# Optimization experiments

Hardware: AMD Instinct MI355X
Metric: run time of the kernel (lower is better)

Reference implementation:

```python
import jax, jax.numpy as jnp
import numpy as np
import math


def setup_inputs() -> dict:
    key = jax.random.key(0)
    ks = jax.random.split(key, 16)
    B, S, H, K, PREV = 32, 2048, 1024, 4, 2
    sc = 0.02
    return {
        "last_hidden": jax.random.normal(ks[0], (1, B, H), jnp.float32),
        "decoder_inputs": jax.random.normal(ks[1], (B, 1, H), jnp.float32),
        "encoder_outputs": jax.random.normal(ks[2], (B, S, H), jnp.float32),
        "attention_scores": jax.random.normal(ks[3], (PREV, B, 1, S), jnp.float32),
        "attention_mask": jnp.zeros((B, 1, S), jnp.float32),
        "evidence_scores": jax.random.uniform(ks[4], (B,), jnp.float32),
        "evidence_sentence_index": jax.random.randint(ks[5], (B, PREV), 0, S, dtype=jnp.int32),
        "W_ih": jax.random.normal(ks[6], (3 * H, H), jnp.float32) * sc,
        "W_hh": jax.random.normal(ks[7], (3 * H, H), jnp.float32) * sc,
        "b_ih": jax.random.normal(ks[8], (3 * H,), jnp.float32) * sc,
        "b_hh": jax.random.normal(ks[9], (3 * H,), jnp.float32) * sc,
        "Wk": jax.random.normal(ks[10], (H, H), jnp.float32) * sc,
        "bk": jnp.zeros((H,), jnp.float32),
        "Wv": jax.random.normal(ks[11], (H, H), jnp.float32) * sc,
        "bv": jnp.zeros((H,), jnp.float32),
        "topk": K,
    }


def _gru_step(x, h, W_ih, W_hh, b_ih, b_hh):
    # x, h: (B, H). PyTorch GRU cell math.
    gi = x @ W_ih.T + b_ih  # (B, 3H)
    gh = h @ W_hh.T + b_hh  # (B, 3H)
    i_r, i_z, i_n = jnp.split(gi, 3, axis=1)
    h_r, h_z, h_n = jnp.split(gh, 3, axis=1)
    r = jax.nn.sigmoid(i_r + h_r)
    z = jax.nn.sigmoid(i_z + h_z)
    n = jnp.tanh(i_n + r * h_n)
    return (1.0 - z) * n + z * h


def reference(last_hidden, decoder_inputs, encoder_outputs, attention_scores,
              attention_mask, evidence_scores, evidence_sentence_index,
              W_ih, W_hh, b_ih, b_hh, Wk, bk, Wv, bv, topk):
    B, S, H = encoder_outputs.shape
    K = topk
    R = B // K  # real batch (beam groups)

    key_eo = encoder_outputs @ Wk.T + bk    # (B, S, H)
    val_eo = encoder_outputs @ Wv.T + bv    # (B, S, H)

    h_new = _gru_step(decoder_inputs[:, 0], last_hidden[0], W_ih, W_hh, b_ih, b_hh)  # (B, H)
    output = h_new[:, None, :]              # (B, 1, H)

    attn_outputs = jnp.einsum('bih,bsh->bis', output, key_eo) / math.sqrt(H) + attention_mask  # (B,1,S)
    attn_alignment = jax.nn.softmax(attn_outputs, axis=-1)
    context = jnp.einsum('bis,bsh->bih', attn_alignment, val_eo)  # (B, 1, H)

    # top-k per beam, then joint rerank over topk*topk candidates per real example
    vals, idx = jax.lax.top_k(attn_alignment.reshape(R, K, S), K)  # (R, K, K), sorted desc
    scores = vals.reshape(B, K)
    sentences = idx.reshape(B, K)
    log_scores = -jnp.log(scores) + evidence_scores[:, None]       # (B, K)

    flat = log_scores.reshape(R, K * K)
    order = jnp.argsort(flat, axis=-1)[:, :K]                      # (R, K) ascending, stable
    new_evidence_scores = jnp.take_along_axis(flat, order, axis=1).reshape(B)
    s_flat = (order // K + jnp.arange(R)[:, None] * K).reshape(B)  # source beam in [0, B)
    r_flat = (order % K).reshape(B)

    sel_sent = sentences[s_flat, r_flat]                           # (B,)
    result = context[s_flat]                                       # (B, 1, H)
    hidden = h_new[s_flat][None]                                   # (1, B, H)
    new_evidence_sentence_index = jnp.concatenate(
        [evidence_sentence_index[s_flat], sel_sent[:, None].astype(evidence_sentence_index.dtype)], axis=1)
    new_attention_scores = jnp.concatenate(
        [attention_scores[:, s_flat], attn_outputs[s_flat][None]], axis=0)  # (prev+1, B, 1, S)
    new_attention_mask = attention_mask[s_flat]                    # (B, 1, S)

    return (result, hidden, new_evidence_sentence_index,
            new_attention_scores, new_attention_mask, new_evidence_scores)
```

## Files before the change

### kernel.cpp

```cpp
#include <hip/hip_runtime.h>
#include <hip/hip_bf16.h>
#include <cfloat>
#include <climits>
#include <cmath>

#define BB 32
#define SS 2048
#define HH 1024
#define KK 4
#define CH 32

__global__ __launch_bounds__(256) void gates_partial(
    const float* __restrict__ x, const float* __restrict__ h_old,
    const float* __restrict__ W_ih, const float* __restrict__ W_hh,
    float* __restrict__ part) {
  int t = threadIdx.x;
  int jb = blockIdx.x;
  int k0 = blockIdx.y * 64;
  bool second = (jb >= 12);
  const float* A = second ? h_old : x;
  const float* W = second ? W_hh : W_ih;
  int j0 = jb * 256;
  int jr = j0 - (second ? 3072 : 0);
  const float* wp = W + (size_t)(jr + t) * HH + k0;
  float acc[32];
#pragma unroll
  for (int b = 0; b < 32; b++) acc[b] = 0.f;
  for (int kk = 0; kk < 64; kk += 4) {
    float4 wv = *(const float4*)(wp + kk);
#pragma unroll
    for (int b = 0; b < 32; b++) {
      float4 a = *(const float4*)(A + (size_t)b * HH + k0 + kk);
      acc[b] += a.x * wv.x + a.y * wv.y + a.z * wv.z + a.w * wv.w;
    }
  }
  float* pb = part + (size_t)blockIdx.y * (32 * 6144) + j0 + t;
#pragma unroll
  for (int b = 0; b < 32; b++) pb[(size_t)b * 6144] = acc[b];
}

__global__ __launch_bounds__(256) void gates_reduce_gru(
    const float* __restrict__ part, const float* __restrict__ b_ih,
    const float* __restrict__ b_hh, const float* __restrict__ h_old,
    float* __restrict__ h_new) {
  int t = threadIdx.x;
  int b = blockIdx.x >> 2;
  int h = (blockIdx.x & 3) * 256 + t;
  float s0 = 0.f, s1 = 0.f, s2 = 0.f, s3 = 0.f, s4 = 0.f, s5 = 0.f;
#pragma unroll
  for (int kc = 0; kc < 16; kc++) {
    const float* p = part + ((size_t)kc * 32 + b) * 6144;
    s0 += p[h];
    s1 += p[1024 + h];
    s2 += p[2048 + h];
    s3 += p[3072 + h];
    s4 += p[4096 + h];
    s5 += p[5120 + h];
  }
  float ir = s0 + b_ih[h], iz = s1 + b_ih[1024 + h], in_ = s2 + b_ih[2048 + h];
  float hr = s3 + b_hh[h], hz = s4 + b_hh[1024 + h], hn = s5 + b_hh[2048 + h];
  float r = 1.f / (1.f + expf(-(ir + hr)));
  float z = 1.f / (1.f + expf(-(iz + hz)));
  float n = tanhf(in_ + r * hn);
  h_new[b * HH + h] = (1.f - z) * n + z * h_old[b * HH + h];
}

__global__ __launch_bounds__(256) void q_partial(const float* __restrict__ hnew,
                                                 const float* __restrict__ Wk,
                                                 float* __restrict__ qpart) {
  int t = threadIdx.x;
  int n0 = blockIdx.x * 512 + 2 * t;
  int k0 = blockIdx.y * 32;
  float acc0[32], acc1[32];
#pragma unroll
  for (int b = 0; b < 32; b++) { acc0[b] = 0.f; acc1[b] = 0.f; }
  for (int k = 0; k < 32; k += 4) {
    float2 w0 = *(const float2*)(Wk + (size_t)(k0 + k) * HH + n0);
    float2 w1 = *(const float2*)(Wk + (size_t)(k0 + k + 1) * HH + n0);
    float2 w2 = *(const float2*)(Wk + (size_t)(k0 + k + 2) * HH + n0);
    float2 w3 = *(const float2*)(Wk + (size_t)(k0 + k + 3) * HH + n0);
#pragma unroll
    for (int b = 0; b < 32; b++) {
      float4 a = *(const float4*)(hnew + (size_t)b * HH + k0 + k);
      acc0[b] += a.x * w0.x + a.y * w1.x + a.z * w2.x + a.w * w3.x;
      acc1[b] += a.x * w0.y + a.y * w1.y + a.z * w2.y + a.w * w3.y;
    }
  }
  float* pb = qpart + (size_t)blockIdx.y * (32 * 1024) + n0;
#pragma unroll
  for (int b = 0; b < 32; b++)
    *(float2*)(pb + (size_t)b * 1024) = make_float2(acc0[b], acc1[b]);
}

__global__ __launch_bounds__(256) void q_reduce_hbk(
    const float* __restrict__ qpart, const float* __restrict__ hnew,
    const float* __restrict__ bk, float* __restrict__ q,
    float* __restrict__ hbk) {
  int t = threadIdx.x;
  if (blockIdx.x < 128) {
    int b = blockIdx.x >> 2;
    int n = (blockIdx.x & 3) * 256 + t;
    float s = 0.f;
#pragma unroll
    for (int kc = 0; kc < 32; kc++) s += qpart[((size_t)kc * 32 + b) * 1024 + n];
    q[b * HH + n] = s;
  } else {
    int w = t >> 6, lane = t & 63;
    const float4* bk4 = (const float4*)bk;
    float4 kv[4];
#pragma unroll
    for (int i = 0; i < 4; i++) kv[i] = bk4[i * 64 + lane];
    for (int b = w; b < BB; b += 4) {
      const float4* h4 = (const float4*)(hnew + (size_t)b * HH);
      float s = 0.f;
#pragma unroll
      for (int i = 0; i < 4; i++) {
        float4 hv = h4[i * 64 + lane];
        s += hv.x * kv[i].x + hv.y * kv[i].y + hv.z * kv[i].z + hv.w * kv[i].w;
      }
#pragma unroll
      for (int off = 32; off; off >>= 1) s += __shfl_xor(s, off);
      if (lane == 0) hbk[b] = s;
    }
  }
}

__global__ __launch_bounds__(256, 4) void fused_attn(
    const float* __restrict__ eo, const float* __restrict__ q,
    const float* __restrict__ hbk, const float* __restrict__ mask,
    float* __restrict__ logits, float* __restrict__ c0part,
    float* __restrict__ msum_part) {
  __shared__ float cacc[4][1024];
  __shared__ float cms[4][2];
  int b = blockIdx.y, sc = blockIdx.x, t = threadIdx.x;
  int w = t >> 6, lane = t & 63;
  const float4* q4 = (const float4*)(q + (size_t)b * HH);
  float4 qv[4];
#pragma unroll
  for (int i = 0; i < 4; i++) qv[i] = q4[i * 64 + lane];
  float hb = hbk[b];
  float m = -FLT_MAX, sum = 0.f;
  float4 acc[4];
#pragma unroll
  for (int i = 0; i < 4; i++) acc[i] = make_float4(0.f, 0.f, 0.f, 0.f);
  int rbase = sc * 64 + w * 16;
  for (int tile = 0; tile < 8; tile++) {
    int r0 = rbase + tile * 2;
    float4 rv[2][4];
#pragma unroll
    for (int rr = 0; rr < 2; rr++) {
      const float4* e4 = (const float4*)(eo + ((size_t)b * SS + r0 + rr) * HH);
#pragma unroll
      for (int i = 0; i < 4; i++) rv[rr][i] = e4[i * 64 + lane];
    }
    float p0 = 0.f, p1 = 0.f;
#pragma unroll
    for (int i = 0; i < 4; i++) {
      p0 += rv[0][i].x * qv[i].x + rv[0][i].y * qv[i].y +
            rv[0][i].z * qv[i].z + rv[0][i].w * qv[i].w;
      p1 += rv[1][i].x * qv[i].x + rv[1][i].y * qv[i].y +
            rv[1][i].z * qv[i].z + rv[1][i].w * qv[i].w;
    }
#pragma unroll
    for (int off = 32; off; off >>= 1) {
      p0 += __shfl_xor(p0, off);
      p1 += __shfl_xor(p1, off);
    }
    float lv0 = (p0 + hb) * 0.03125f + mask[(size_t)b * SS + r0];
    float lv1 = (p1 + hb) * 0.03125f + mask[(size_t)b * SS + r0 + 1];
    if (lane == 0) {
      logits[(size_t)b * SS + r0] = lv0;
      logits[(size_t)b * SS + r0 + 1] = lv1;
    }
    float m_new = fmaxf(m, fmaxf(lv0, lv1));
    float scale = expf(m - m_new);
    float w0 = expf(lv0 - m_new), w1 = expf(lv1 - m_new);
    sum = sum * scale + w0 + w1;
#pragma unroll
    for (int i = 0; i < 4; i++) {
      acc[i].x = acc[i].x * scale + w0 * rv[0][i].x + w1 * rv[1][i].x;
      acc[i].y = acc[i].y * scale + w0 * rv[0][i].y + w1 * rv[1][i].y;
      acc[i].z = acc[i].z * scale + w0 * rv[0][i].z + w1 * rv[1][i].z;
      acc[i].w = acc[i].w * scale + w0 * rv[0][i].w + w1 * rv[1][i].w;
    }
    m = m_new;
  }
#pragma unroll
  for (int i = 0; i < 4; i++)
    *(float4*)&cacc[w][i * 256 + lane * 4] = acc[i];
  if (lane == 0) { cms[w][0] = m; cms[w][1] = sum; }
  __syncthreads();
  float m0 = cms[0][0], m1 = cms[1][0], m2 = cms[2][0], m3 = cms[3][0];
  float mb = fmaxf(fmaxf(m0, m1), fmaxf(m2, m3));
  float wt0 = expf(m0 - mb), wt1 = expf(m1 - mb), wt2 = expf(m2 - mb),
        wt3 = expf(m3 - mb);
  float sb = cms[0][1] * wt0 + cms[1][1] * wt1 + cms[2][1] * wt2 + cms[3][1] * wt3;
  float4 a0 = *(float4*)&cacc[0][4 * t];
  float4 a1 = *(float4*)&cacc[1][4 * t];
  float4 a2 = *(float4*)&cacc[2][4 * t];
  float4 a3 = *(float4*)&cacc[3][4 * t];
  float4 r;
  r.x = wt0 * a0.x + wt1 * a1.x + wt2 * a2.x + wt3 * a3.x;
  r.y = wt0 * a0.y + wt1 * a1.y + wt2 * a2.y + wt3 * a3.y;
  r.z = wt0 * a0.z + wt1 * a1.z + wt2 * a2.z + wt3 * a3.z;
  r.w = wt0 * a0.w + wt1 * a1.w + wt2 * a2.w + wt3 * a3.w;
  *(float4*)(c0part + ((size_t)sc * 32 + b) * 1024 + 4 * t) = r;
  if (t == 0) {
    msum_part[((size_t)sc * 32 + b) * 2 + 0] = mb;
    msum_part[((size_t)sc * 32 + b) * 2 + 1] = sb;
  }
}

__device__ __forceinline__ bool vi_better(float av, int ai, float bv, int bi) {
  return av > bv || (av == bv && ai < bi);
}

__global__ __launch_bounds__(256) void attn_finish(
    const float* __restrict__ c0part, const float* __restrict__ msum_part,
    const float* __restrict__ logits, float* __restrict__ c0,
    float* __restrict__ scores, int* __restrict__ sent) {
  int b = blockIdx.x, t = threadIdx.x;
  float m = -FLT_MAX;
  float ms[CH];
#pragma unroll
  for (int c = 0; c < CH; c++) {
    ms[c] = msum_part[((size_t)c * 32 + b) * 2 + 0];
    m = fmaxf(m, ms[c]);
  }
  float sum = 0.f;
  float wc[CH];
#pragma unroll
  for (int c = 0; c < CH; c++) {
    wc[c] = expf(ms[c] - m);
    sum += msum_part[((size_t)c * 32 + b) * 2 + 1] * wc[c];
  }
  float inv = 1.f / sum;
  float4 a = make_float4(0.f, 0.f, 0.f, 0.f);
#pragma unroll
  for (int c = 0; c < CH; c++) {
    float4 v = *(const float4*)(c0part + ((size_t)c * 32 + b) * 1024 + 4 * t);
    a.x += wc[c] * v.x; a.y += wc[c] * v.y;
    a.z += wc[c] * v.z; a.w += wc[c] * v.w;
  }
  a.x *= inv; a.y *= inv; a.z *= inv; a.w *= inv;
  *(float4*)(c0 + (size_t)b * HH + 4 * t) = a;

  float tv0 = -FLT_MAX, tv1 = -FLT_MAX, tv2 = -FLT_MAX, tv3 = -FLT_MAX;
  int ti0 = INT_MAX, ti1 = INT_MAX, ti2 = INT_MAX, ti3 = INT_MAX;
#pragma unroll
  for (int it = 0; it < 8; it++) {
    int idx = it * 256 + t;
    float v = logits[(size_t)b * SS + idx];
    if (vi_better(v, idx, tv3, ti3)) {
      tv3 = v; ti3 = idx;
      if (vi_better(tv3, ti3, tv2, ti2)) { float fv = tv2; int fi = ti2; tv2 = tv3; ti2 = ti3; tv3 = fv; ti3 = fi; }
      if (vi_better(tv2, ti2, tv1, ti1)) { float fv = tv1; int fi = ti1; tv1 = tv2; ti1 = ti2; tv2 = fv; ti2 = fi; }
      if (vi_better(tv1, ti1, tv0, ti0)) { float fv = tv0; int fi = ti0; tv0 = tv1; ti0 = ti1; tv1 = fv; ti1 = fi; }
    }
  }
  __shared__ float sv[256][4];
  __shared__ int si[256][4];
  sv[t][0] = tv0; sv[t][1] = tv1; sv[t][2] = tv2; sv[t][3] = tv3;
  si[t][0] = ti0; si[t][1] = ti1; si[t][2] = ti2; si[t][3] = ti3;
  __syncthreads();
  for (int off = 128; off; off >>= 1) {
    if (t < off) {
      float bv0 = sv[t + off][0], bv1 = sv[t + off][1], bv2 = sv[t + off][2], bv3 = sv[t + off][3];
      int bi0 = si[t + off][0], bi1 = si[t + off][1], bi2 = si[t + off][2], bi3 = si[t + off][3];
      float mv0, mv1, mv2, mv3; int mi0, mi1, mi2, mi3;
      if (vi_better(tv0, ti0, bv3, bi3)) { mv0 = tv0; mi0 = ti0; } else { mv0 = bv3; mi0 = bi3; }
      if (vi_better(tv1, ti1, bv2, bi2)) { mv1 = tv1; mi1 = ti1; } else { mv1 = bv2; mi1 = bi2; }
      if (vi_better(tv2, ti2, bv1, bi1)) { mv2 = tv2; mi2 = ti2; } else { mv2 = bv1; mi2 = bi1; }
      if (vi_better(tv3, ti3, bv0, bi0)) { mv3 = tv3; mi3 = ti3; } else { mv3 = bv0; mi3 = bi0; }
      if (!vi_better(mv0, mi0, mv2, mi2)) { float fv = mv0; int fi = mi0; mv0 = mv2; mi0 = mi2; mv2 = fv; mi2 = fi; }
      if (!vi_better(mv1, mi1, mv3, mi3)) { float fv = mv1; int fi = mi1; mv1 = mv3; mi1 = mi3; mv3 = fv; mi3 = fi; }
      if (!vi_better(mv0, mi0, mv1, mi1)) { float fv = mv0; int fi = mi0; mv0 = mv1; mi0 = mi1; mv1 = fv; mi1 = fi; }
      if (!vi_better(mv2, mi2, mv3, mi3)) { float fv = mv2; int fi = mi2; mv2 = mv3; mi2 = mi3; mv3 = fv; mi3 = fi; }
      tv0 = mv0; tv1 = mv1; tv2 = mv2; tv3 = mv3;
      ti0 = mi0; ti1 = mi1; ti2 = mi2; ti3 = mi3;
      sv[t][0] = tv0; sv[t][1] = tv1; sv[t][2] = tv2; sv[t][3] = tv3;
      si[t][0] = ti0; si[t][1] = ti1; si[t][2] = ti2; si[t][3] = ti3;
    }
    __syncthreads();
  }
  if (t == 0) {
    scores[b * KK + 0] = expf(tv0 - m) * inv; sent[b * KK + 0] = ti0;
    scores[b * KK + 1] = expf(tv1 - m) * inv; sent[b * KK + 1] = ti1;
    scores[b * KK + 2] = expf(tv2 - m) * inv; sent[b * KK + 2] = ti2;
    scores[b * KK + 3] = expf(tv3 - m) * inv; sent[b * KK + 3] = ti3;
  }
}

__global__ __launch_bounds__(256) void ctx_partial(const float* __restrict__ c0,
                                                   const float* __restrict__ Wv,
                                                   float* __restrict__ part) {
  int t = threadIdx.x;
  int j = blockIdx.x * 256 + t;
  int k0 = blockIdx.y * 32;
  const float* wp = Wv + (size_t)j * HH + k0;
  float acc[32];
#pragma unroll
  for (int b = 0; b < 32; b++) acc[b] = 0.f;
  for (int kk = 0; kk < 32; kk += 4) {
    float4 wv = *(const float4*)(wp + kk);
#pragma unroll
    for (int b = 0; b < 32; b++) {
      float4 a = *(const float4*)(c0 + (size_t)b * HH + k0 + kk);
      acc[b] += a.x * wv.x + a.y * wv.y + a.z * wv.z + a.w * wv.w;
    }
  }
  float* pb = part + (size_t)blockIdx.y * (32 * 1024) + j;
#pragma unroll
  for (int b = 0; b < 32; b++) pb[(size_t)b * 1024] = acc[b];
}

__global__ __launch_bounds__(256) void sel_gather(
    const float* __restrict__ scores, const int* __restrict__ sent,
    const float* __restrict__ evidence, const int* __restrict__ esi,
    const float* __restrict__ ctxpart, const float* __restrict__ bv,
    const float* __restrict__ hnew, const float* __restrict__ attn_in,
    const float* __restrict__ logits, const float* __restrict__ mask,
    float* __restrict__ out0, float* __restrict__ out1,
    float* __restrict__ out2, float* __restrict__ out3,
    float* __restrict__ out4, float* __restrict__ out5) {
  __shared__ int s_sh;
  int b = blockIdx.x, t = threadIdx.x;
  if (t == 0) {
    int r = b >> 2, j = b & 3;
    float ls[16];
    bool used[16];
    for (int k1 = 0; k1 < 4; k1++)
      for (int k2 = 0; k2 < 4; k2++)
        ls[k1 * 4 + k2] = -logf(scores[(r * 4 + k1) * 4 + k2]) + evidence[r * 4 + k1];
    for (int i = 0; i < 16; i++) used[i] = false;
    int best = 0;
    float bvv = FLT_MAX;
    for (int jj = 0; jj <= j; jj++) {
      best = 0;
      bvv = FLT_MAX;
      for (int i = 0; i < 16; i++)
        if (!used[i] && ls[i] < bvv) { bvv = ls[i]; best = i; }
      used[best] = true;
    }
    int k1 = best >> 2, k2 = best & 3;
    int sSel = r * 4 + k1;
    s_sh = sSel;
    out5[b] = bvv;
    out2[b * 3 + 0] = (float)esi[sSel * 2 + 0];
    out2[b * 3 + 1] = (float)esi[sSel * 2 + 1];
    out2[b * 3 + 2] = (float)sent[sSel * 4 + k2];
  }
  __syncthreads();
  int s = s_sh;
  {
    float4 s0 = ((const float4*)bv)[t];
#pragma unroll
    for (int kc = 0; kc < 32; kc++) {
      float4 v = *(const float4*)(ctxpart + ((size_t)kc * 32 + s) * 1024 + 4 * t);
      s0.x += v.x; s0.y += v.y; s0.z += v.z; s0.w += v.w;
    }
    ((float4*)(out0 + (size_t)b * HH))[t] = s0;
    ((float4*)(out1 + (size_t)b * HH))[t] =
        ((const float4*)(hnew + (size_t)s * HH))[t];
  }
#pragma unroll
  for (int p = 0; p < 2; p++) {
    const float4* src = (const float4*)(attn_in + ((size_t)p * BB + s) * SS);
    float4* dst = (float4*)(out3 + ((size_t)p * BB + b) * SS);
    dst[t] = src[t];
    dst[t + 256] = src[t + 256];
  }
  {
    const float4* lg = (const float4*)(logits + (size_t)s * SS);
    float4* d2 = (float4*)(out3 + ((size_t)2 * BB + b) * SS);
    d2[t] = lg[t];
    d2[t + 256] = lg[t + 256];
    const float4* mk = (const float4*)(mask + (size_t)s * SS);
    float4* d4 = (float4*)(out4 + (size_t)b * SS);
    d4[t] = mk[t];
    d4[t + 256] = mk[t + 256];
  }
}

extern "C" void kernel_launch(void* const* d_in, const int* in_sizes, int n_in,
                              void* d_out, int out_size, void* d_ws, size_t ws_size,
                              hipStream_t stream) {
  const float* h_old = (const float*)d_in[0];
  const float* x     = (const float*)d_in[1];
  const float* eo    = (const float*)d_in[2];
  const float* attn_in = (const float*)d_in[3];
  const float* mask  = (const float*)d_in[4];
  const float* evidence = (const float*)d_in[5];
  const int*   esi   = (const int*)d_in[6];
  const float* W_ih  = (const float*)d_in[7];
  const float* W_hh  = (const float*)d_in[8];
  const float* b_ih  = (const float*)d_in[9];
  const float* b_hh  = (const float*)d_in[10];
  const float* Wk    = (const float*)d_in[11];
  const float* bk    = (const float*)d_in[12];
  const float* Wv    = (const float*)d_in[13];
  const float* bv    = (const float*)d_in[14];

  float* w = (float*)d_ws;
  float* h_new  = w + 0;
  float* q      = w + 32768;
  float* hbk    = w + 65536;
  float* logits = w + 65568;
  float* scores = w + 131104;
  int*   sent   = (int*)(w + 131232);
  float* c0     = w + 131360;
  float* msum_part = w + 164128;
  float* c0part = w + 166176;
  float* gpart  = w + 1214752;
  float* qpart  = w + 4360480;
  float* ctxpart= w + 5409056;

  float* out0 = (float*)d_out;
  float* out1 = out0 + 32768;
  float* out2 = out1 + 32768;
  float* out3 = out2 + 96;
  float* out4 = out3 + 196608;
  float* out5 = out4 + 65536;

  gates_partial<<<dim3(24, 16), 256, 0, stream>>>(x, h_old, W_ih, W_hh, gpart);
  gates_reduce_gru<<<128, 256, 0, stream>>>(gpart, b_ih, b_hh, h_old, h_new);
  q_partial<<<dim3(2, 32), 256, 0, stream>>>(h_new, Wk, qpart);
  q_reduce_hbk<<<129, 256, 0, stream>>>(qpart, h_new, bk, q, hbk);
  fused_attn<<<dim3(CH, BB), 256, 0, stream>>>(eo, q, hbk, mask, logits, c0part, msum_part);
  attn_finish<<<BB, 256, 0, stream>>>(c0part, msum_part, logits, c0, scores, sent);
  ctx_partial<<<dim3(4, 32), 256, 0, stream>>>(c0, Wv, ctxpart);
  sel_gather<<<BB, 256, 0, stream>>>(scores, sent, evidence, esi, ctxpart, bv,
                                     h_new, attn_in, logits, mask,
                                     out0, out1, out2, out3, out4, out5);
}
```

Before: 153.6 us.

## Fuse GRU with query projection, fold q-reduce into attention, fuse ctx GEMV into gather

Merges the GRU reduction with the Wk query projection into one kernel that writes 4 per-chunk partials. The q reduction and the h·bk bias dot now happen at the start of fused_attn, staged through LDS. The context Wv projection is computed only for each selected beam inside the gather kernel, which replaces a separate all-batch GEMV and its partial reduction. The attention loop is also software-pipelined with double-buffered row tiles. Together this cuts the launch count from 8 to 5 and removes intermediate partial buffers. The cost is that fused_attn reads the q partials redundantly in every block, and the per-beam Wv GEMV reads Wv once per output beam.

New measurement: 238.7 us. 55.5% more time.

```diff
diff --git a/kernel.cpp b/kernel.cpp
--- a/kernel.cpp
+++ b/kernel.cpp
@@ -39,17 +39,19 @@
   for (int b = 0; b < 32; b++) pb[(size_t)b * 6144] = acc[b];
 }
 
-__global__ __launch_bounds__(256) void gates_reduce_gru(
+__global__ __launch_bounds__(256) void gru_q(
     const float* __restrict__ part, const float* __restrict__ b_ih,
     const float* __restrict__ b_hh, const float* __restrict__ h_old,
-    float* __restrict__ h_new) {
+    const float* __restrict__ Wk, float* __restrict__ h_new,
+    float* __restrict__ qpart2) {
+  __shared__ float hs[256];
   int t = threadIdx.x;
-  int b = blockIdx.x >> 2;
-  int h = (blockIdx.x & 3) * 256 + t;
+  int kc = blockIdx.x, b = blockIdx.y;
+  int h = kc * 256 + t;
   float s0 = 0.f, s1 = 0.f, s2 = 0.f, s3 = 0.f, s4 = 0.f, s5 = 0.f;
 #pragma unroll
-  for (int kc = 0; kc < 16; kc++) {
-    const float* p = part + ((size_t)kc * 32 + b) * 6144;
+  for (int c = 0; c < 16; c++) {
+    const float* p = part + ((size_t)c * 32 + b) * 6144;
     s0 += p[h];
     s1 += p[1024 + h];
     s2 += p[2048 + h];
@@ -62,132 +64,123 @@
   float r = 1.f / (1.f + expf(-(ir + hr)));
   float z = 1.f / (1.f + expf(-(iz + hz)));
   float n = tanhf(in_ + r * hn);
-  h_new[b * HH + h] = (1.f - z) * n + z * h_old[b * HH + h];
-}
-
-__global__ __launch_bounds__(256) void q_partial(const float* __restrict__ hnew,
-                                                 const float* __restrict__ Wk,
-                                                 float* __restrict__ qpart) {
-  int t = threadIdx.x;
-  int n0 = blockIdx.x * 512 + 2 * t;
-  int k0 = blockIdx.y * 32;
-  float acc0[32], acc1[32];
-#pragma unroll
-  for (int b = 0; b < 32; b++) { acc0[b] = 0.f; acc1[b] = 0.f; }
-  for (int k = 0; k < 32; k += 4) {
-    float2 w0 = *(const float2*)(Wk + (size_t)(k0 + k) * HH + n0);
-    float2 w1 = *(const float2*)(Wk + (size_t)(k0 + k + 1) * HH + n0);
-    float2 w2 = *(const float2*)(Wk + (size_t)(k0 + k + 2) * HH + n0);
-    float2 w3 = *(const float2*)(Wk + (size_t)(k0 + k + 3) * HH + n0);
-#pragma unroll
-    for (int b = 0; b < 32; b++) {
-      float4 a = *(const float4*)(hnew + (size_t)b * HH + k0 + k);
-      acc0[b] += a.x * w0.x + a.y * w1.x + a.z * w2.x + a.w * w3.x;
-      acc1[b] += a.x * w0.y + a.y * w1.y + a.z * w2.y + a.w * w3.y;
-    }
-  }
-  float* pb = qpart + (size_t)blockIdx.y * (32 * 1024) + n0;
-#pragma unroll
-  for (int b = 0; b < 32; b++)
-    *(float2*)(pb + (size_t)b * 1024) = make_float2(acc0[b], acc1[b]);
-}
-
-__global__ __launch_bounds__(256) void q_reduce_hbk(
-    const float* __restrict__ qpart, const float* __restrict__ hnew,
-    const float* __restrict__ bk, float* __restrict__ q,
-    float* __restrict__ hbk) {
-  int t = threadIdx.x;
-  if (blockIdx.x < 128) {
-    int b = blockIdx.x >> 2;
-    int n = (blockIdx.x & 3) * 256 + t;
-    float s = 0.f;
-#pragma unroll
-    for (int kc = 0; kc < 32; kc++) s += qpart[((size_t)kc * 32 + b) * 1024 + n];
-    q[b * HH + n] = s;
-  } else {
-    int w = t >> 6, lane = t & 63;
-    const float4* bk4 = (const float4*)bk;
-    float4 kv[4];
-#pragma unroll
-    for (int i = 0; i < 4; i++) kv[i] = bk4[i * 64 + lane];
-    for (int b = w; b < BB; b += 4) {
-      const float4* h4 = (const float4*)(hnew + (size_t)b * HH);
-      float s = 0.f;
-#pragma unroll
-      for (int i = 0; i < 4; i++) {
-        float4 hv = h4[i * 64 + lane];
-        s += hv.x * kv[i].x + hv.y * kv[i].y + hv.z * kv[i].z + hv.w * kv[i].w;
-      }
-#pragma unroll
-      for (int off = 32; off; off >>= 1) s += __shfl_xor(s, off);
-      if (lane == 0) hbk[b] = s;
-    }
-  }
+  float hv = (1.f - z) * n + z * h_old[b * HH + h];
+  h_new[b * HH + h] = hv;
+  hs[t] = hv;
+  __syncthreads();
+  float4 acc = make_float4(0.f, 0.f, 0.f, 0.f);
+  const float* wbase = Wk + (size_t)kc * 256 * HH + 4 * t;
+  for (int k = 0; k < 256; k += 4) {
+    float4 w0 = *(const float4*)(wbase + (size_t)(k + 0) * HH);
+    float4 w1 = *(const float4*)(wbase + (size_t)(k + 1) * HH);
+    float4 w2 = *(const float4*)(wbase + (size_t)(k + 2) * HH);
+    float4 w3 = *(const float4*)(wbase + (size_t)(k + 3) * HH);
+    float a0 = hs[k], a1 = hs[k + 1], a2 = hs[k + 2], a3 = hs[k + 3];
+    acc.x += a0 * w0.x + a1 * w1.x + a2 * w2.x + a3 * w3.x;
+    acc.y += a0 * w0.y + a1 * w1.y + a2 * w2.y + a3 * w3.y;
+    acc.z += a0 * w0.z + a1 * w1.z + a2 * w2.z + a3 * w3.z;
+    acc.w += a0 * w0.w + a1 * w1.w + a2 * w2.w + a3 * w3.w;
+  }
+  *(float4*)(qpart2 + ((size_t)b * 4 + kc) * HH + 4 * t) = acc;
+}
+
+__device__ __forceinline__ void attn_load_tile(float4 (&rv)[2][4],
+                                               const float* __restrict__ eo,
+                                               int b, int r0, int lane) {
+#pragma unroll
+  for (int rr = 0; rr < 2; rr++) {
+    const float4* e4 = (const float4*)(eo + ((size_t)b * SS + r0 + rr) * HH);
+#pragma unroll
+    for (int i = 0; i < 4; i++) rv[rr][i] = e4[i * 64 + lane];
+  }
+}
+
+__device__ __forceinline__ void attn_process_tile(
+    const float4 (&rv)[2][4], const float4 (&qv)[4], float hb,
+    const float* __restrict__ mask, float* __restrict__ logits, int b, int r0,
+    int lane, float& m, float& sum, float4 (&acc)[4]) {
+  float p0 = 0.f, p1 = 0.f;
+#pragma unroll
+  for (int i = 0; i < 4; i++) {
+    p0 += rv[0][i].x * qv[i].x + rv[0][i].y * qv[i].y +
+          rv[0][i].z * qv[i].z + rv[0][i].w * qv[i].w;
+    p1 += rv[1][i].x * qv[i].x + rv[1][i].y * qv[i].y +
+          rv[1][i].z * qv[i].z + rv[1][i].w * qv[i].w;
+  }
+#pragma unroll
+  for (int off = 32; off; off >>= 1) {
+    p0 += __shfl_xor(p0, off);
+    p1 += __shfl_xor(p1, off);
+  }
+  float lv0 = (p0 + hb) * 0.03125f + mask[(size_t)b * SS + r0];
+  float lv1 = (p1 + hb) * 0.03125f + mask[(size_t)b * SS + r0 + 1];
+  if (lane == 0) {
+    logits[(size_t)b * SS + r0] = lv0;
+    logits[(size_t)b * SS + r0 + 1] = lv1;
+  }
+  float m_new = fmaxf(m, fmaxf(lv0, lv1));
+  float scale = expf(m - m_new);
+  float w0 = expf(lv0 - m_new), w1 = expf(lv1 - m_new);
+  sum = sum * scale + w0 + w1;
+#pragma unroll
+  for (int i = 0; i < 4; i++) {
+    acc[i].x = acc[i].x * scale + w0 * rv[0][i].x + w1 * rv[1][i].x;
+    acc[i].y = acc[i].y * scale + w0 * rv[0][i].y + w1 * rv[1][i].y;
+    acc[i].z = acc[i].z * scale + w0 * rv[0][i].z + w1 * rv[1][i].z;
+    acc[i].w = acc[i].w * scale + w0 * rv[0][i].w + w1 * rv[1][i].w;
+  }
+  m = m_new;
 }
 
 __global__ __launch_bounds__(256, 4) void fused_attn(
-    const float* __restrict__ eo, const float* __restrict__ q,
-    const float* __restrict__ hbk, const float* __restrict__ mask,
-    float* __restrict__ logits, float* __restrict__ c0part,
-    float* __restrict__ msum_part) {
+    const float* __restrict__ eo, const float* __restrict__ qpart2,
+    const float* __restrict__ h_new, const float* __restrict__ bk,
+    const float* __restrict__ mask, float* __restrict__ logits,
+    float* __restrict__ c0part, float* __restrict__ msum_part) {
+  __shared__ float q_lds[HH];
+  __shared__ float wred[4];
   __shared__ float cacc[4][1024];
   __shared__ float cms[4][2];
   int b = blockIdx.y, sc = blockIdx.x, t = threadIdx.x;
   int w = t >> 6, lane = t & 63;
-  const float4* q4 = (const float4*)(q + (size_t)b * HH);
+  {
+    float4 qs = *(const float4*)(qpart2 + ((size_t)b * 4 + 0) * HH + 4 * t);
+#pragma unroll
+    for (int kc = 1; kc < 4; kc++) {
+      float4 v = *(const float4*)(qpart2 + ((size_t)b * 4 + kc) * HH + 4 * t);
+      qs.x += v.x; qs.y += v.y; qs.z += v.z; qs.w += v.w;
+    }
+    *(float4*)&q_lds[4 * t] = qs;
+    float4 hv = *(const float4*)(h_new + (size_t)b * HH + 4 * t);
+    float4 kv = *(const float4*)(bk + 4 * t);
+    float p = hv.x * kv.x + hv.y * kv.y + hv.z * kv.z + hv.w * kv.w;
+#pragma unroll
+    for (int off = 32; off; off >>= 1) p += __shfl_xor(p, off);
+    if (lane == 0) wred[w] = p;
+  }
+  __syncthreads();
+  float hb = wred[0] + wred[1] + wred[2] + wred[3];
   float4 qv[4];
 #pragma unroll
-  for (int i = 0; i < 4; i++) qv[i] = q4[i * 64 + lane];
-  float hb = hbk[b];
+  for (int i = 0; i < 4; i++) qv[i] = *(const float4*)&q_lds[(i * 64 + lane) * 4];
+
   float m = -FLT_MAX, sum = 0.f;
   float4 acc[4];
 #pragma unroll
   for (int i = 0; i < 4; i++) acc[i] = make_float4(0.f, 0.f, 0.f, 0.f);
   int rbase = sc * 64 + w * 16;
-  for (int tile = 0; tile < 8; tile++) {
-    int r0 = rbase + tile * 2;
-    float4 rv[2][4];
-#pragma unroll
-    for (int rr = 0; rr < 2; rr++) {
-      const float4* e4 = (const float4*)(eo + ((size_t)b * SS + r0 + rr) * HH);
-#pragma unroll
-      for (int i = 0; i < 4; i++) rv[rr][i] = e4[i * 64 + lane];
-    }
-    float p0 = 0.f, p1 = 0.f;
-#pragma unroll
-    for (int i = 0; i < 4; i++) {
-      p0 += rv[0][i].x * qv[i].x + rv[0][i].y * qv[i].y +
-            rv[0][i].z * qv[i].z + rv[0][i].w * qv[i].w;
-      p1 += rv[1][i].x * qv[i].x + rv[1][i].y * qv[i].y +
-            rv[1][i].z * qv[i].z + rv[1][i].w * qv[i].w;
-    }
-#pragma unroll
-    for (int off = 32; off; off >>= 1) {
-      p0 += __shfl_xor(p0, off);
-      p1 += __shfl_xor(p1, off);
-    }
-    float lv0 = (p0 + hb) * 0.03125f + mask[(size_t)b * SS + r0];
-    float lv1 = (p1 + hb) * 0.03125f + mask[(size_t)b * SS + r0 + 1];
-    if (lane == 0) {
-      logits[(size_t)b * SS + r0] = lv0;
-      logits[(size_t)b * SS + r0 + 1] = lv1;
-    }
-    float m_new = fmaxf(m, fmaxf(lv0, lv1));
-    float scale = expf(m - m_new);
-    float w0 = expf(lv0 - m_new), w1 = expf(lv1 - m_new);
-    sum = sum * scale + w0 + w1;
-#pragma unroll
-    for (int i = 0; i < 4; i++) {
-      acc[i].x = acc[i].x * scale + w0 * rv[0][i].x + w1 * rv[1][i].x;
-      acc[i].y = acc[i].y * scale + w0 * rv[0][i].y + w1 * rv[1][i].y;
-      acc[i].z = acc[i].z * scale + w0 * rv[0][i].z + w1 * rv[1][i].z;
-      acc[i].w = acc[i].w * scale + w0 * rv[0][i].w + w1 * rv[1][i].w;
-    }
-    m = m_new;
-  }
-#pragma unroll
-  for (int i = 0; i < 4; i++)
-    *(float4*)&cacc[w][i * 256 + lane * 4] = acc[i];
+  float4 rvA[2][4], rvB[2][4];
+  attn_load_tile(rvA, eo, b, rbase, lane);
+#pragma unroll 1
+  for (int it = 0; it < 4; it++) {
+    int r0 = rbase + it * 4;
+    attn_load_tile(rvB, eo, b, r0 + 2, lane);
+    attn_process_tile(rvA, qv, hb, mask, logits, b, r0, lane, m, sum, acc);
+    if (it < 3) attn_load_tile(rvA, eo, b, r0 + 4, lane);
+    attn_process_tile(rvB, qv, hb, mask, logits, b, r0 + 2, lane, m, sum, acc);
+  }
+#pragma unroll
+  for (int i = 0; i < 4; i++) *(float4*)&cacc[w][i * 256 + lane * 4] = acc[i];
   if (lane == 0) { cms[w][0] = m; cms[w][1] = sum; }
   __syncthreads();
   float m0 = cms[0][0], m1 = cms[1][0], m2 = cms[2][0], m3 = cms[3][0];
@@ -291,40 +284,19 @@
   }
 }
 
-__global__ __launch_bounds__(256) void ctx_partial(const float* __restrict__ c0,
-                                                   const float* __restrict__ Wv,
-                                                   float* __restrict__ part) {
-  int t = threadIdx.x;
-  int j = blockIdx.x * 256 + t;
-  int k0 = blockIdx.y * 32;
-  const float* wp = Wv + (size_t)j * HH + k0;
-  float acc[32];
-#pragma unroll
-  for (int b = 0; b < 32; b++) acc[b] = 0.f;
-  for (int kk = 0; kk < 32; kk += 4) {
-    float4 wv = *(const float4*)(wp + kk);
-#pragma unroll
-    for (int b = 0; b < 32; b++) {
-      float4 a = *(const float4*)(c0 + (size_t)b * HH + k0 + kk);
-      acc[b] += a.x * wv.x + a.y * wv.y + a.z * wv.z + a.w * wv.w;
-    }
-  }
-  float* pb = part + (size_t)blockIdx.y * (32 * 1024) + j;
-#pragma unroll
-  for (int b = 0; b < 32; b++) pb[(size_t)b * 1024] = acc[b];
-}
-
-__global__ __launch_bounds__(256) void sel_gather(
+__global__ __launch_bounds__(256) void ctx_sel_gather(
     const float* __restrict__ scores, const int* __restrict__ sent,
     const float* __restrict__ evidence, const int* __restrict__ esi,
-    const float* __restrict__ ctxpart, const float* __restrict__ bv,
-    const float* __restrict__ hnew, const float* __restrict__ attn_in,
-    const float* __restrict__ logits, const float* __restrict__ mask,
-    float* __restrict__ out0, float* __restrict__ out1,
-    float* __restrict__ out2, float* __restrict__ out3,
-    float* __restrict__ out4, float* __restrict__ out5) {
+    const float* __restrict__ Wv, const float* __restrict__ bvec,
+    const float* __restrict__ c0, const float* __restrict__ hnew,
+    const float* __restrict__ attn_in, const float* __restrict__ logits,
+    const float* __restrict__ mask, float* __restrict__ out0,
+    float* __restrict__ out1, float* __restrict__ out2,
+    float* __restrict__ out3, float* __restrict__ out4,
+    float* __restrict__ out5) {
   __shared__ int s_sh;
-  int b = blockIdx.x, t = threadIdx.x;
+  int jq = blockIdx.x, b = blockIdx.y, t = threadIdx.x;
+  int w = t >> 6, lane = t & 63;
   if (t == 0) {
     int r = b >> 2, j = b & 3;
     float ls[16];
@@ -345,41 +317,43 @@
     int k1 = best >> 2, k2 = best & 3;
     int sSel = r * 4 + k1;
     s_sh = sSel;
-    out5[b] = bvv;
-    out2[b * 3 + 0] = (float)esi[sSel * 2 + 0];
-    out2[b * 3 + 1] = (float)esi[sSel * 2 + 1];
-    out2[b * 3 + 2] = (float)sent[sSel * 4 + k2];
+    if (jq == 0) {
+      out5[b] = bvv;
+      out2[b * 3 + 0] = (float)esi[sSel * 2 + 0];
+      out2[b * 3 + 1] = (float)esi[sSel * 2 + 1];
+      out2[b * 3 + 2] = (float)sent[sSel * 4 + k2];
+    }
   }
   __syncthreads();
   int s = s_sh;
-  {
-    float4 s0 = ((const float4*)bv)[t];
-#pragma unroll
-    for (int kc = 0; kc < 32; kc++) {
-      float4 v = *(const float4*)(ctxpart + ((size_t)kc * 32 + s) * 1024 + 4 * t);
-      s0.x += v.x; s0.y += v.y; s0.z += v.z; s0.w += v.w;
-    }
-    ((float4*)(out0 + (size_t)b * HH))[t] = s0;
-    ((float4*)(out1 + (size_t)b * HH))[t] =
-        ((const float4*)(hnew + (size_t)s * HH))[t];
-  }
+  float4 cv[4];
+  const float4* c4 = (const float4*)(c0 + (size_t)s * HH);
+#pragma unroll
+  for (int i = 0; i < 4; i++) cv[i] = c4[i * 64 + lane];
+  int jbase = jq * 256 + w * 64;
+  for (int rr = 0; rr < 64; rr++) {
+    int j = jbase + rr;
+    const float4* w4 = (const float4*)(Wv + (size_t)j * HH);
+    float p = 0.f;
+#pragma unroll
+    for (int i = 0; i < 4; i++) {
+      float4 wv = w4[i * 64 + lane];
+      p += wv.x * cv[i].x + wv.y * cv[i].y + wv.z * cv[i].z + wv.w * cv[i].w;
+    }
+#pragma unroll
+    for (int off = 32; off; off >>= 1) p += __shfl_xor(p, off);
+    if (lane == 0) out0[(size_t)b * HH + j] = p + bvec[j];
+  }
+  out1[(size_t)b * HH + jq * 256 + t] = hnew[(size_t)s * HH + jq * 256 + t];
 #pragma unroll
   for (int p = 0; p < 2; p++) {
-    const float4* src = (const float4*)(attn_in + ((size_t)p * BB + s) * SS);
-    float4* dst = (float4*)(out3 + ((size_t)p * BB + b) * SS);
-    dst[t] = src[t];
-    dst[t + 256] = src[t + 256];
-  }
-  {
-    const float4* lg = (const float4*)(logits + (size_t)s * SS);
-    float4* d2 = (float4*)(out3 + ((size_t)2 * BB + b) * SS);
-    d2[t] = lg[t];
-    d2[t + 256] = lg[t + 256];
-    const float4* mk = (const float4*)(mask + (size_t)s * SS);
-    float4* d4 = (float4*)(out4 + (size_t)b * SS);
-    d4[t] = mk[t];
-    d4[t + 256] = mk[t + 256];
-  }
+    *(float2*)(out3 + ((size_t)p * BB + b) * SS + jq * 512 + 2 * t) =
+        *(const float2*)(attn_in + ((size_t)p * BB + s) * SS + jq * 512 + 2 * t);
+  }
+  *(float2*)(out3 + ((size_t)2 * BB + b) * SS + jq * 512 + 2 * t) =
+      *(const float2*)(logits + (size_t)s * SS + jq * 512 + 2 * t);
+  *(float2*)(out4 + (size_t)b * SS + jq * 512 + 2 * t) =
+      *(const float2*)(mask + (size_t)s * SS + jq * 512 + 2 * t);
 }
 
 extern "C" void kernel_launch(void* const* d_in, const int* in_sizes, int n_in,
@@ -403,17 +377,14 @@
 
   float* w = (float*)d_ws;
   float* h_new  = w + 0;
-  float* q      = w + 32768;
-  float* hbk    = w + 65536;
-  float* logits = w + 65568;
-  float* scores = w + 131104;
-  int*   sent   = (int*)(w + 131232);
-  float* c0     = w + 131360;
-  float* msum_part = w + 164128;
-  float* c0part = w + 166176;
-  float* gpart  = w + 1214752;
-  float* qpart  = w + 4360480;
-  float* ctxpart= w + 5409056;
+  float* logits = w + 32768;
+  float* scores = w + 98304;
+  int*   sent   = (int*)(w + 98432);
+  float* c0     = w + 98560;
+  float* msum_part = w + 131328;
+  float* c0part = w + 133376;
+  float* gpart  = w + 1181952;
+  float* qpart2 = w + 4327680;
 
   float* out0 = (float*)d_out;
   float* out1 = out0 + 32768;
@@ -423,13 +394,11 @@
   float* out5 = out4 + 65536;
 
   gates_partial<<<dim3(24, 16), 256, 0, stream>>>(x, h_old, W_ih, W_hh, gpart);
-  gates_reduce_gru<<<128, 256, 0, stream>>>(gpart, b_ih, b_hh, h_old, h_new);
-  q_partial<<<dim3(2, 32), 256, 0, stream>>>(h_new, Wk, qpart);
-  q_reduce_hbk<<<129, 256, 0, stream>>>(qpart, h_new, bk, q, hbk);
-  fused_attn<<<dim3(CH, BB), 256, 0, stream>>>(eo, q, hbk, mask, logits, c0part, msum_part);
+  gru_q<<<dim3(4, 32), 256, 0, stream>>>(gpart, b_ih, b_hh, h_old, Wk, h_new, qpart2);
+  fused_attn<<<dim3(CH, BB), 256, 0, stream>>>(eo, qpart2, h_new, bk, mask,
+                                               logits, c0part, msum_part);
   attn_finish<<<BB, 256, 0, stream>>>(c0part, msum_part, logits, c0, scores, sent);
-  ctx_partial<<<dim3(4, 32), 256, 0, stream>>>(c0, Wv, ctxpart);
-  sel_gather<<<BB, 256, 0, stream>>>(scores, sent, evidence, esi, ctxpart, bv,
-                                     h_new, attn_in, logits, mask,
-                                     out0, out1, out2, out3, out4, out5);
-}
+  ctx_sel_gather<<<dim3(4, BB), 256, 0, stream>>>(
+      scores, sent, evidence, esi, Wv, bv, c0, h_new, attn_in, logits, mask,
+      out0, out1, out2, out3, out4, out5);
+}
```

## Widen grids for small GEMV kernels and fuse context projection into gather

Applied to the files above, without the earlier changes.

Splits the GRU gate GEMV over twice as many K chunks and reshapes the Wk query GEMV grid, both to spread the small matrix-vector work across more blocks. The c0 reduction in attn_finish now gets 128 extra blocks. The ctx_partial kernel is removed: each output beam's context projection through Wv is computed directly inside the gather kernel, over a 2D grid, for the selected source beam only. This saves one launch and the partial buffer, but the top-k selection is recomputed in every block and Wv rows are read once per batch element.

After: 177.4 us. 15.5% more time.

```diff
diff --git a/kernel.cpp b/kernel.cpp
--- a/kernel.cpp
+++ b/kernel.cpp
@@ -16,7 +16,7 @@
     float* __restrict__ part) {
   int t = threadIdx.x;
   int jb = blockIdx.x;
-  int k0 = blockIdx.y * 64;
+  int k0 = blockIdx.y * 32;
   bool second = (jb >= 12);
   const float* A = second ? h_old : x;
   const float* W = second ? W_hh : W_ih;
@@ -26,7 +26,8 @@
   float acc[32];
 #pragma unroll
   for (int b = 0; b < 32; b++) acc[b] = 0.f;
-  for (int kk = 0; kk < 64; kk += 4) {
+#pragma unroll
+  for (int kk = 0; kk < 32; kk += 4) {
     float4 wv = *(const float4*)(wp + kk);
 #pragma unroll
     for (int b = 0; b < 32; b++) {
@@ -39,17 +40,17 @@
   for (int b = 0; b < 32; b++) pb[(size_t)b * 6144] = acc[b];
 }
 
-__global__ __launch_bounds__(256) void gates_reduce_gru(
+__global__ __launch_bounds__(256) void gru_pw(
     const float* __restrict__ part, const float* __restrict__ b_ih,
     const float* __restrict__ b_hh, const float* __restrict__ h_old,
     float* __restrict__ h_new) {
   int t = threadIdx.x;
-  int b = blockIdx.x >> 2;
-  int h = (blockIdx.x & 3) * 256 + t;
+  int b = blockIdx.x;
+  int h = blockIdx.y * 256 + t;
   float s0 = 0.f, s1 = 0.f, s2 = 0.f, s3 = 0.f, s4 = 0.f, s5 = 0.f;
 #pragma unroll
-  for (int kc = 0; kc < 16; kc++) {
-    const float* p = part + ((size_t)kc * 32 + b) * 6144;
+  for (int c = 0; c < 32; c++) {
+    const float* p = part + ((size_t)c * 32 + b) * 6144;
     s0 += p[h];
     s1 += p[1024 + h];
     s2 += p[2048 + h];
@@ -69,27 +70,26 @@
                                                  const float* __restrict__ Wk,
                                                  float* __restrict__ qpart) {
   int t = threadIdx.x;
-  int n0 = blockIdx.x * 512 + 2 * t;
-  int k0 = blockIdx.y * 32;
-  float acc0[32], acc1[32];
-#pragma unroll
-  for (int b = 0; b < 32; b++) { acc0[b] = 0.f; acc1[b] = 0.f; }
+  int n = blockIdx.y * 256 + t;
+  int k0 = blockIdx.x * 32;
+  float acc[32];
+#pragma unroll
+  for (int b = 0; b < 32; b++) acc[b] = 0.f;
+#pragma unroll
   for (int k = 0; k < 32; k += 4) {
-    float2 w0 = *(const float2*)(Wk + (size_t)(k0 + k) * HH + n0);
-    float2 w1 = *(const float2*)(Wk + (size_t)(k0 + k + 1) * HH + n0);
-    float2 w2 = *(const float2*)(Wk + (size_t)(k0 + k + 2) * HH + n0);
-    float2 w3 = *(const float2*)(Wk + (size_t)(k0 + k + 3) * HH + n0);
+    float w0 = Wk[(size_t)(k0 + k) * HH + n];
+    float w1 = Wk[(size_t)(k0 + k + 1) * HH + n];
+    float w2 = Wk[(size_t)(k0 + k + 2) * HH + n];
+    float w3 = Wk[(size_t)(k0 + k + 3) * HH + n];
 #pragma unroll
     for (int b = 0; b < 32; b++) {
       float4 a = *(const float4*)(hnew + (size_t)b * HH + k0 + k);
-      acc0[b] += a.x * w0.x + a.y * w1.x + a.z * w2.x + a.w * w3.x;
-      acc1[b] += a.x * w0.y + a.y * w1.y + a.z * w2.y + a.w * w3.y;
-    }
-  }
-  float* pb = qpart + (size_t)blockIdx.y * (32 * 1024) + n0;
-#pragma unroll
-  for (int b = 0; b < 32; b++)
-    *(float2*)(pb + (size_t)b * 1024) = make_float2(acc0[b], acc1[b]);
+      acc[b] += a.x * w0 + a.y * w1 + a.z * w2 + a.w * w3;
+    }
+  }
+  float* pb = qpart + (size_t)blockIdx.x * (32 * 1024) + n;
+#pragma unroll
+  for (int b = 0; b < 32; b++) pb[(size_t)b * 1024] = acc[b];
 }
 
 __global__ __launch_bounds__(256) void q_reduce_hbk(
@@ -125,7 +125,7 @@
   }
 }
 
-__global__ __launch_bounds__(256, 4) void fused_attn(
+__global__ __launch_bounds__(256) void fused_attn(
     const float* __restrict__ eo, const float* __restrict__ q,
     const float* __restrict__ hbk, const float* __restrict__ mask,
     float* __restrict__ logits, float* __restrict__ c0part,
@@ -186,8 +186,7 @@
     m = m_new;
   }
 #pragma unroll
-  for (int i = 0; i < 4; i++)
-    *(float4*)&cacc[w][i * 256 + lane * 4] = acc[i];
+  for (int i = 0; i < 4; i++) *(float4*)&cacc[w][i * 256 + lane * 4] = acc[i];
   if (lane == 0) { cms[w][0] = m; cms[w][1] = sum; }
   __syncthreads();
   float m0 = cms[0][0], m1 = cms[1][0], m2 = cms[2][0], m3 = cms[3][0];
@@ -219,7 +218,8 @@
     const float* __restrict__ c0part, const float* __restrict__ msum_part,
     const float* __restrict__ logits, float* __restrict__ c0,
     float* __restrict__ scores, int* __restrict__ sent) {
-  int b = blockIdx.x, t = threadIdx.x;
+  int bid = blockIdx.x, t = threadIdx.x;
+  int b = (bid < 128) ? (bid >> 2) : (bid - 128);
   float m = -FLT_MAX;
   float ms[CH];
 #pragma unroll
@@ -235,15 +235,16 @@
     sum += msum_part[((size_t)c * 32 + b) * 2 + 1] * wc[c];
   }
   float inv = 1.f / sum;
-  float4 a = make_float4(0.f, 0.f, 0.f, 0.f);
-#pragma unroll
-  for (int c = 0; c < CH; c++) {
-    float4 v = *(const float4*)(c0part + ((size_t)c * 32 + b) * 1024 + 4 * t);
-    a.x += wc[c] * v.x; a.y += wc[c] * v.y;
-    a.z += wc[c] * v.z; a.w += wc[c] * v.w;
-  }
-  a.x *= inv; a.y *= inv; a.z *= inv; a.w *= inv;
-  *(float4*)(c0 + (size_t)b * HH + 4 * t) = a;
+
+  if (bid < 128) {
+    int h = (bid & 3) * 256 + t;
+    float a = 0.f;
+#pragma unroll
+    for (int c = 0; c < CH; c++)
+      a += wc[c] * c0part[((size_t)c * 32 + b) * 1024 + h];
+    c0[(size_t)b * HH + h] = a * inv;
+    return;
+  }
 
   float tv0 = -FLT_MAX, tv1 = -FLT_MAX, tv2 = -FLT_MAX, tv3 = -FLT_MAX;
   int ti0 = INT_MAX, ti1 = INT_MAX, ti2 = INT_MAX, ti3 = INT_MAX;
@@ -291,40 +292,19 @@
   }
 }
 
-__global__ __launch_bounds__(256) void ctx_partial(const float* __restrict__ c0,
-                                                   const float* __restrict__ Wv,
-                                                   float* __restrict__ part) {
-  int t = threadIdx.x;
-  int j = blockIdx.x * 256 + t;
-  int k0 = blockIdx.y * 32;
-  const float* wp = Wv + (size_t)j * HH + k0;
-  float acc[32];
-#pragma unroll
-  for (int b = 0; b < 32; b++) acc[b] = 0.f;
-  for (int kk = 0; kk < 32; kk += 4) {
-    float4 wv = *(const float4*)(wp + kk);
-#pragma unroll
-    for (int b = 0; b < 32; b++) {
-      float4 a = *(const float4*)(c0 + (size_t)b * HH + k0 + kk);
-      acc[b] += a.x * wv.x + a.y * wv.y + a.z * wv.z + a.w * wv.w;
-    }
-  }
-  float* pb = part + (size_t)blockIdx.y * (32 * 1024) + j;
-#pragma unroll
-  for (int b = 0; b < 32; b++) pb[(size_t)b * 1024] = acc[b];
-}
-
-__global__ __launch_bounds__(256) void sel_gather(
+__global__ __launch_bounds__(256) void ctx_sel_gather(
     const float* __restrict__ scores, const int* __restrict__ sent,
     const float* __restrict__ evidence, const int* __restrict__ esi,
-    const float* __restrict__ ctxpart, const float* __restrict__ bv,
-    const float* __restrict__ hnew, const float* __restrict__ attn_in,
-    const float* __restrict__ logits, const float* __restrict__ mask,
-    float* __restrict__ out0, float* __restrict__ out1,
-    float* __restrict__ out2, float* __restrict__ out3,
-    float* __restrict__ out4, float* __restrict__ out5) {
+    const float* __restrict__ Wv, const float* __restrict__ bvec,
+    const float* __restrict__ c0, const float* __restrict__ hnew,
+    const float* __restrict__ attn_in, const float* __restrict__ logits,
+    const float* __restrict__ mask, float* __restrict__ out0,
+    float* __restrict__ out1, float* __restrict__ out2,
+    float* __restrict__ out3, float* __restrict__ out4,
+    float* __restrict__ out5) {
   __shared__ int s_sh;
-  int b = blockIdx.x, t = threadIdx.x;
+  int jo = blockIdx.x, b = blockIdx.y, t = threadIdx.x;
+  int w = t >> 6, lane = t & 63;
   if (t == 0) {
     int r = b >> 2, j = b & 3;
     float ls[16];
@@ -345,41 +325,59 @@
     int k1 = best >> 2, k2 = best & 3;
     int sSel = r * 4 + k1;
     s_sh = sSel;
-    out5[b] = bvv;
-    out2[b * 3 + 0] = (float)esi[sSel * 2 + 0];
-    out2[b * 3 + 1] = (float)esi[sSel * 2 + 1];
-    out2[b * 3 + 2] = (float)sent[sSel * 4 + k2];
+    if (jo == 0) {
+      out5[b] = bvv;
+      out2[b * 3 + 0] = (float)esi[sSel * 2 + 0];
+      out2[b * 3 + 1] = (float)esi[sSel * 2 + 1];
+      out2[b * 3 + 2] = (float)sent[sSel * 4 + k2];
+    }
   }
   __syncthreads();
   int s = s_sh;
-  {
-    float4 s0 = ((const float4*)bv)[t];
-#pragma unroll
-    for (int kc = 0; kc < 32; kc++) {
-      float4 v = *(const float4*)(ctxpart + ((size_t)kc * 32 + s) * 1024 + 4 * t);
-      s0.x += v.x; s0.y += v.y; s0.z += v.z; s0.w += v.w;
-    }
-    ((float4*)(out0 + (size_t)b * HH))[t] = s0;
-    ((float4*)(out1 + (size_t)b * HH))[t] =
-        ((const float4*)(hnew + (size_t)s * HH))[t];
-  }
-#pragma unroll
-  for (int p = 0; p < 2; p++) {
-    const float4* src = (const float4*)(attn_in + ((size_t)p * BB + s) * SS);
-    float4* dst = (float4*)(out3 + ((size_t)p * BB + b) * SS);
-    dst[t] = src[t];
-    dst[t + 256] = src[t + 256];
-  }
-  {
-    const float4* lg = (const float4*)(logits + (size_t)s * SS);
-    float4* d2 = (float4*)(out3 + ((size_t)2 * BB + b) * SS);
-    d2[t] = lg[t];
-    d2[t + 256] = lg[t + 256];
-    const float4* mk = (const float4*)(mask + (size_t)s * SS);
-    float4* d4 = (float4*)(out4 + (size_t)b * SS);
-    d4[t] = mk[t];
-    d4[t + 256] = mk[t + 256];
-  }
+  float4 cv[4];
+  const float4* c4 = (const float4*)(c0 + (size_t)s * HH);
+#pragma unroll
+  for (int i = 0; i < 4; i++) cv[i] = c4[i * 64 + lane];
+  int jbase = jo * 128 + w * 32;
+  for (int rb = 0; rb < 32; rb += 4) {
+    float4 wv[4][4];
+#pragma unroll
+    for (int rr = 0; rr < 4; rr++) {
+      const float4* w4 = (const float4*)(Wv + (size_t)(jbase + rb + rr) * HH);
+#pragma unroll
+      for (int i = 0; i < 4; i++) wv[rr][i] = w4[i * 64 + lane];
+    }
+    float p[4];
+#pragma unroll
+    for (int rr = 0; rr < 4; rr++) {
+      float s_ = 0.f;
+#pragma unroll
+      for (int i = 0; i < 4; i++) {
+        s_ += wv[rr][i].x * cv[i].x + wv[rr][i].y * cv[i].y +
+              wv[rr][i].z * cv[i].z + wv[rr][i].w * cv[i].w;
+      }
+      p[rr] = s_;
+    }
+#pragma unroll
+    for (int off = 32; off; off >>= 1) {
+#pragma unroll
+      for (int rr = 0; rr < 4; rr++) p[rr] += __shfl_xor(p[rr], off);
+    }
+    if (lane == 0) {
+#pragma unroll
+      for (int rr = 0; rr < 4; rr++) {
+        int j = jbase + rb + rr;
+        out0[(size_t)b * HH + j] = p[rr] + bvec[j];
+      }
+    }
+  }
+  if (t < 128) out1[(size_t)b * HH + jo * 128 + t] = hnew[(size_t)s * HH + jo * 128 + t];
+  int col = jo * 256 + t;
+#pragma unroll
+  for (int p = 0; p < 2; p++)
+    out3[((size_t)p * BB + b) * SS + col] = attn_in[((size_t)p * BB + s) * SS + col];
+  out3[((size_t)2 * BB + b) * SS + col] = logits[(size_t)s * SS + col];
+  out4[(size_t)b * SS + col] = mask[(size_t)s * SS + col];
 }
 
 extern "C" void kernel_launch(void* const* d_in, const int* in_sizes, int n_in,
@@ -412,8 +410,7 @@
   float* msum_part = w + 164128;
   float* c0part = w + 166176;
   float* gpart  = w + 1214752;
-  float* qpart  = w + 4360480;
-  float* ctxpart= w + 5409056;
+  float* qpart  = w + 7506208;
 
   float* out0 = (float*)d_out;
   float* out1 = out0 + 32768;
@@ -422,14 +419,14 @@
   float* out4 = out3 + 196608;
   float* out5 = out4 + 65536;
 
-  gates_partial<<<dim3(24, 16), 256, 0, stream>>>(x, h_old, W_ih, W_hh, gpart);
-  gates_reduce_gru<<<128, 256, 0, stream>>>(gpart, b_ih, b_hh, h_old, h_new);
-  q_partial<<<dim3(2, 32), 256, 0, stream>>>(h_new, Wk, qpart);
+  gates_partial<<<dim3(24, 32), 256, 0, stream>>>(x, h_old, W_ih, W_hh, gpart);
+  gru_pw<<<dim3(32, 4), 256, 0, stream>>>(gpart, b_ih, b_hh, h_old, h_new);
+  q_partial<<<dim3(32, 4), 256, 0, stream>>>(h_new, Wk, qpart);
   q_reduce_hbk<<<129, 256, 0, stream>>>(qpart, h_new, bk, q, hbk);
-  fused_attn<<<dim3(CH, BB), 256, 0, stream>>>(eo, q, hbk, mask, logits, c0part, msum_part);
-  attn_finish<<<BB, 256, 0, stream>>>(c0part, msum_part, logits, c0, scores, sent);
-  ctx_partial<<<dim3(4, 32), 256, 0, stream>>>(c0, Wv, ctxpart);
-  sel_gather<<<BB, 256, 0, stream>>>(scores, sent, evidence, esi, ctxpart, bv,
-                                     h_new, attn_in, logits, mask,
-                                     out0, out1, out2, out3, out4, out5);
-}
+  fused_attn<<<dim3(CH, BB), 256, 0, stream>>>(eo, q, hbk, mask, logits,
+                                               c0part, msum_part);
+  attn_finish<<<160, 256, 0, stream>>>(c0part, msum_part, logits, c0, scores, sent);
+  ctx_sel_gather<<<dim3(8, BB), 256, 0, stream>>>(
+      scores, sent, evidence, esi, Wv, bv, c0, h_new, attn_in, logits, mask,
+      out0, out1, out2, out3, out4, out5);
+}
```
